# Optimization experiments

Measured on AMD Instinct MI355X. Metric: run time of the kernel, lower is better.

Reference implementation:

```python
import jax, jax.numpy as jnp
import numpy as np

B, N, E, D, H, C, FF, NQ, NCLS = 4, 1024, 512, 256, 2, 128, 1024, 4, 24
K_LOCAL, K_GLOBAL = 8, 7


def _ln(x, g, b, eps=1e-5):
    m = jnp.mean(x, -1, keepdims=True)
    v = jnp.mean((x - m) ** 2, -1, keepdims=True)
    return (x - m) * jax.lax.rsqrt(v + eps) * g + b


def _knn_mask(dist, k, exclude_self):
    # dist: [n, n]; returns bool mask[target, source] of k nearest sources per target
    n = dist.shape[-1]
    d = jnp.where(jnp.eye(n, dtype=bool), 1e9, dist) if exclude_self else dist
    idx = jax.lax.top_k(-d, k)[1]  # [n, k]
    rows = jnp.arange(n)[:, None]
    return jnp.zeros((n, n), dtype=bool).at[rows, idx].set(True)


def _mha(q, k, v, scale, extra_mask=None):
    # q: [B,Lq,H,C]  k,v: [B,Lk,H,C]
    logits = jnp.einsum('bqhc,bkhc->bhqk', q, k) * scale
    if extra_mask is not None:
        logits = logits + extra_mask
    a = jax.nn.softmax(logits, axis=-1)
    return jnp.einsum('bhqk,bkhc->bqhc', a, v)


def _forward(inputs, cellposes, sparse_rand, emb_W, emb_b, pe_tab, pe_W1, pe_b1, pe_W2, pe_b2,
             gat_W, gat_att_src, gat_att_dst, gat_b, ln_g, ln_b,
             tf_qkv_W, tf_qkv_b, tf_out_W, tf_out_b, tf_ff1_W, tf_ff1_b, tf_ff2_W, tf_ff2_b,
             tf_ln1_g, tf_ln1_b, tf_ln2_g, tf_ln2_b,
             query_embed, pool_in_W, pool_in_b, pool_out_W, pool_out_b,
             m1_W, m1_b, m_ln1_g, m_ln1_b, m2_W, m2_b, m_ln2_g, m_ln2_b, m3_W, m3_b,
             c1_W, c1_b, c2_W, c2_b, c3_W, c3_b, c4_W, c4_b, masks):
    # masks are all ones (full bags) -> key_padding_mask is all-False, no padding effect
    x = inputs @ emb_W.T + emb_b                                  # [B,N,D]
    # 2D position embedding: per-coordinate Embedding -> Linear -> ReLU -> Linear
    pos_idx = jnp.clip(cellposes, 0, 1000).astype(jnp.int32)      # [B,N,2]
    pes = []
    for c in range(2):
        e = pe_tab[c][pos_idx[..., c]]                            # [B,N,D//2]
        e = jax.nn.relu(e @ pe_W1[c].T + pe_b1[c]) @ pe_W2[c].T + pe_b2[c]
        pes.append(e)
    x = x + jnp.concatenate(pes, axis=-1)
    # kNN graph: local k=8 with self-loops + global k=7 without; coalesce('max') => edge-set union
    pm = cellposes.mean(axis=1, keepdims=True)
    ps = cellposes.std(axis=1, keepdims=True) + 1e-8
    pn = (cellposes - pm) / ps
    sq = jnp.sum((pn[:, :, None, :] - pn[:, None, :, :]) ** 2, axis=-1)
    dist = jax.lax.stop_gradient(jnp.sqrt(sq + 1e-12))            # [B,N,N]
    local = jax.vmap(lambda d: _knn_mask(d, K_LOCAL, False))(dist)
    glob = jax.vmap(lambda d: _knn_mask(d, K_GLOBAL, True))(dist)
    adj = local | glob                                            # [B, target, source]
    # GAT layers (PyG GATConv; edge weights are ignored since edge_dim=None)
    for l in range(gat_W.shape[0]):
        res = x
        h = (x @ gat_W[l].T).reshape(B, N, H, C)
        a_src = jnp.einsum('bnhc,hc->bnh', h, gat_att_src[l])
        a_dst = jnp.einsum('bnhc,hc->bnh', h, gat_att_dst[l])
        e = jax.nn.leaky_relu(a_dst[:, :, None, :] + a_src[:, None, :, :], 0.2)  # [B,t,s,H]
        e = jnp.where(adj[..., None], e, -1e9)
        a = jax.nn.softmax(e, axis=2)
        out = jnp.einsum('btsh,bshc->bthc', a, h).reshape(B, N, D) + gat_b[l]
        x = _ln(out + res, ln_g, ln_b)
    # TransformerEncoder: post-norm, ReLU FFN, batch_first, eval (no dropout)
    scale = 1.0 / jnp.sqrt(jnp.float32(C))
    for l in range(tf_qkv_W.shape[0]):
        qkv = x @ tf_qkv_W[l].T + tf_qkv_b[l]
        q, k, v = [t.reshape(B, N, H, C) for t in jnp.split(qkv, 3, axis=-1)]
        o = _mha(q, k, v, scale).reshape(B, N, D) @ tf_out_W[l].T + tf_out_b[l]
        x = _ln(x + o, tf_ln1_g[l], tf_ln1_b[l])
        ff = jax.nn.relu(x @ tf_ff1_W[l].T + tf_ff1_b[l]) @ tf_ff2_W[l].T + tf_ff2_b[l]
        x = _ln(x + ff, tf_ln2_g[l], tf_ln2_b[l])
    x = _ln(x, ln_g, ln_b)
    pooled_avg = x.mean(axis=1)                                   # AdaptiveAvgPool1d(1) == mean over seq
    # Sparse multihead attention pooling with learned queries
    queries = jnp.broadcast_to(query_embed[None], (B, NQ, D))
    attn_mask = jnp.where(sparse_rand < 0.3, 0.0, -1e9)           # [NQ, N]
    Wq, Wk, Wv = jnp.split(pool_in_W, 3, axis=0)
    bq, bk, bv = jnp.split(pool_in_b, 3, axis=0)
    q = (queries @ Wq.T + bq).reshape(B, NQ, H, C)
    k = (x @ Wk.T + bk).reshape(B, N, H, C)
    v = (x @ Wv.T + bv).reshape(B, N, H, C)
    pooled_att = _mha(q, k, v, scale, attn_mask[None, None]).reshape(B, NQ, D) @ pool_out_W.T + pool_out_b
    combined = jnp.concatenate([pooled_avg, pooled_att.reshape(B, NQ * D)], axis=-1)  # [B,(1+NQ)*D]
    h = jax.nn.relu(combined @ m1_W.T + m1_b)
    h = _ln(h, m_ln1_g, m_ln1_b)
    h = jax.nn.relu(h @ m2_W.T + m2_b)
    h = _ln(h, m_ln2_g, m_ln2_b)
    h = h @ m3_W.T + m3_b
    h = jax.nn.relu(h @ c1_W.T + c1_b)
    h = jax.nn.relu(h @ c2_W.T + c2_b)
    h = jax.nn.relu(h @ c3_W.T + c3_b)
    return h @ c4_W.T + c4_b                                      # [B, num_classes]


def setup_inputs() -> dict:
    key = jax.random.key(0)
    ks = iter(jax.random.split(key, 80))
    def W(shape, s=0.02):
        return jax.random.normal(next(ks), shape, jnp.float32) * s
    z = lambda *s: jnp.zeros(s, jnp.float32)
    o = lambda *s: jnp.ones(s, jnp.float32)
    return dict(
        inputs=jax.random.normal(next(ks), (B, N, E), jnp.float32),
        cellposes=jax.random.uniform(next(ks), (B, N, 2), jnp.float32) * 1000.0,
        sparse_rand=jax.random.uniform(next(ks), (NQ, N), jnp.float32),
        emb_W=W((D, E)), emb_b=z(D),
        pe_tab=W((2, 1001, D // 2)), pe_W1=W((2, D // 2, D // 2)), pe_b1=z(2, D // 2),
        pe_W2=W((2, D // 2, D // 2)), pe_b2=z(2, D // 2),
        gat_W=W((2, D, D)), gat_att_src=W((2, H, C)), gat_att_dst=W((2, H, C)), gat_b=z(2, D),
        ln_g=o(D), ln_b=z(D),
        tf_qkv_W=W((2, 3 * D, D)), tf_qkv_b=z(2, 3 * D), tf_out_W=W((2, D, D)), tf_out_b=z(2, D),
        tf_ff1_W=W((2, FF, D)), tf_ff1_b=z(2, FF), tf_ff2_W=W((2, D, FF)), tf_ff2_b=z(2, D),
        tf_ln1_g=o(2, D), tf_ln1_b=z(2, D), tf_ln2_g=o(2, D), tf_ln2_b=z(2, D),
        query_embed=W((NQ, D)),
        pool_in_W=W((3 * D, D)), pool_in_b=z(3 * D), pool_out_W=W((D, D)), pool_out_b=z(D),
        m1_W=W((1024, (1 + NQ) * D)), m1_b=z(1024), m_ln1_g=o(1024), m_ln1_b=z(1024),
        m2_W=W((1024, 1024)), m2_b=z(1024), m_ln2_g=o(1024), m_ln2_b=z(1024),
        m3_W=W((1024, 1024)), m3_b=z(1024),
        c1_W=W((1032, 1024)), c1_b=z(1032), c2_W=W((512, 1032)), c2_b=z(512),
        c3_W=W((256, 512)), c3_b=z(256), c4_W=W((NCLS, 256)), c4_b=z(NCLS),
        masks=jnp.ones((B, N), jnp.int32),
    )


def reference(inputs, cellposes, sparse_rand, emb_W, emb_b, pe_tab, pe_W1, pe_b1, pe_W2, pe_b2,
              gat_W, gat_att_src, gat_att_dst, gat_b, ln_g, ln_b,
              tf_qkv_W, tf_qkv_b, tf_out_W, tf_out_b, tf_ff1_W, tf_ff1_b, tf_ff2_W, tf_ff2_b,
              tf_ln1_g, tf_ln1_b, tf_ln2_g, tf_ln2_b,
              query_embed, pool_in_W, pool_in_b, pool_out_W, pool_out_b,
              m1_W, m1_b, m_ln1_g, m_ln1_b, m2_W, m2_b, m_ln2_g, m_ln2_b, m3_W, m3_b,
              c1_W, c1_b, c2_W, c2_b, c3_W, c3_b, c4_W, c4_b, masks):
    return _forward(inputs, cellposes, sparse_rand, emb_W, emb_b, pe_tab, pe_W1, pe_b1, pe_W2, pe_b2,
                    gat_W, gat_att_src, gat_att_dst, gat_b, ln_g, ln_b,
                    tf_qkv_W, tf_qkv_b, tf_out_W, tf_out_b, tf_ff1_W, tf_ff1_b, tf_ff2_W, tf_ff2_b,
                    tf_ln1_g, tf_ln1_b, tf_ln2_g, tf_ln2_b,
                    query_embed, pool_in_W, pool_in_b, pool_out_W, pool_out_b,
                    m1_W, m1_b, m_ln1_g, m_ln1_b, m2_W, m2_b, m_ln2_g, m_ln2_b, m3_W, m3_b,
                    c1_W, c1_b, c2_W, c2_b, c3_W, c3_b, c4_W, c4_b, masks)
```

## Files before the change

kernel.cpp:

```cpp
#include <hip/hip_runtime.h>
#include <hip/hip_bf16.h>


typedef __bf16 bf16x8 __attribute__((ext_vector_type(8)));
typedef float  f32x4  __attribute__((ext_vector_type(4)));

__device__ __forceinline__ ushort f2b(float f) {
  __hip_bfloat16 h = __float2bfloat16(f);
  return *(ushort*)&h;
}
__device__ __forceinline__ float b2f(ushort u) {
  union { unsigned i; float f; } v; v.i = ((unsigned)u) << 16; return v.f;
}

__device__ __forceinline__ float blk_sum256(float v, float* red) {
  int t = threadIdx.x;
  red[t] = v; __syncthreads();
  #pragma unroll
  for (int off = 128; off > 0; off >>= 1) {
    if (t < off) red[t] += red[t + off];
    __syncthreads();
  }
  float r = red[0]; __syncthreads();
  return r;
}

__device__ __forceinline__ void stage8(const ushort* __restrict__ src, ushort* dst) {
  *(uint4*)dst = *(const uint4*)src;
}
__device__ __forceinline__ void stage8(const float* __restrict__ src, ushort* dst) {
  float4 a = ((const float4*)src)[0];
  float4 b = ((const float4*)src)[1];
  ushort4 o0, o1;
  o0.x = f2b(a.x); o0.y = f2b(a.y); o0.z = f2b(a.z); o0.w = f2b(a.w);
  o1.x = f2b(b.x); o1.y = f2b(b.y); o1.z = f2b(b.z); o1.w = f2b(b.w);
  *(ushort4*)dst = o0;
  *(ushort4*)(dst + 4) = o1;
}

template<typename CT, typename AT, typename WT, bool VSPLIT, bool GATS>
__global__ __launch_bounds__(256) void mfma_gemm(
    const AT* __restrict__ A, int lda,
    const WT* __restrict__ Bw, int ldb,
    const float* __restrict__ bias,
    CT* __restrict__ C, int ldc, int K, int relu,
    ushort* __restrict__ VT,
    const float* __restrict__ asrcW, const float* __restrict__ adstW,
    float* __restrict__ ASRC, float* __restrict__ ADST)
{
  __shared__ ushort As[64][40];
  __shared__ ushort Bs[128][40];
  int tid = threadIdx.x;
  int lane = tid & 63, wave = tid >> 6;
  int wm = wave >> 1, wn = wave & 1;
  int quad = lane >> 4, l16 = lane & 15;
  long mBase = blockIdx.y * 64, nBase = blockIdx.x * 128;

  f32x4 zero4 = {0.f, 0.f, 0.f, 0.f};
  f32x4 acc[2][4];
  #pragma unroll
  for (int i = 0; i < 2; i++)
    #pragma unroll
    for (int j = 0; j < 4; j++) acc[i][j] = zero4;

  for (int k0 = 0; k0 < K; k0 += 32) {
    {
      int r = tid >> 2, sg = (tid & 3) * 8;
      stage8(A + (mBase + r) * lda + k0 + sg, &As[r][sg]);
    }
    #pragma unroll
    for (int p = 0; p < 2; p++) {
      int idx = p * 256 + tid;
      int r = idx >> 2, sg = (idx & 3) * 8;
      stage8(Bw + (nBase + r) * ldb + k0 + sg, &Bs[r][sg]);
    }
    __syncthreads();
    bf16x8 af[2], bfr[4];
    #pragma unroll
    for (int i = 0; i < 2; i++)
      af[i] = *(const bf16x8*)&As[wm * 32 + i * 16 + l16][quad * 8];
    #pragma unroll
    for (int j = 0; j < 4; j++)
      bfr[j] = *(const bf16x8*)&Bs[wn * 64 + j * 16 + l16][quad * 8];
    #pragma unroll
    for (int i = 0; i < 2; i++)
      #pragma unroll
      for (int j = 0; j < 4; j++)
        acc[i][j] = __builtin_amdgcn_mfma_f32_16x16x32_bf16(af[i], bfr[j], acc[i][j], 0, 0, 0);
    __syncthreads();
  }
  #pragma unroll
  for (int i = 0; i < 2; i++) {
    #pragma unroll
    for (int j = 0; j < 4; j++) {
      long col = nBase + wn * 64 + j * 16 + l16;
      float bv = bias ? bias[col] : 0.f;
      long row0 = mBase + wm * 32 + i * 16 + quad * 4;
      if (VSPLIT && col >= 512) {
        int cm = (int)col - 512, hh = cm >> 7, cc = cm & 127;
        long bidx = row0 >> 10, n0 = row0 & 1023;
        ushort4 o;
        o.x = f2b(acc[i][j][0] + bv);
        o.y = f2b(acc[i][j][1] + bv);
        o.z = f2b(acc[i][j][2] + bv);
        o.w = f2b(acc[i][j][3] + bv);
        *(ushort4*)&VT[(((bidx * 2 + hh) * 128 + cc) << 10) + n0] = o;
      } else {
        #pragma unroll
        for (int r = 0; r < 4; r++) {
          float v = acc[i][j][r] + bv;
          if (relu) v = fmaxf(v, 0.f);
          if constexpr (sizeof(CT) == 2) C[(row0 + r) * ldc + col] = f2b(v);
          else                           C[(row0 + r) * ldc + col] = v;
        }
      }
    }
  }
  if constexpr (GATS) {
    __shared__ float RS[64][2], RD[64][2];
    float ps[2][4], pd[2][4];
    #pragma unroll
    for (int i = 0; i < 2; i++)
      #pragma unroll
      for (int r = 0; r < 4; r++) { ps[i][r] = 0.f; pd[i][r] = 0.f; }
    #pragma unroll
    for (int j = 0; j < 4; j++) {
      long col = nBase + wn * 64 + j * 16 + l16;
      float ws = asrcW[col], wd = adstW[col];
      #pragma unroll
      for (int i = 0; i < 2; i++)
        #pragma unroll
        for (int r = 0; r < 4; r++) {
          ps[i][r] += acc[i][j][r] * ws;
          pd[i][r] += acc[i][j][r] * wd;
        }
    }
    #pragma unroll
    for (int off = 1; off < 16; off <<= 1)
      #pragma unroll
      for (int i = 0; i < 2; i++)
        #pragma unroll
        for (int r = 0; r < 4; r++) {
          ps[i][r] += __shfl_xor(ps[i][r], off);
          pd[i][r] += __shfl_xor(pd[i][r], off);
        }
    if (l16 == 0) {
      #pragma unroll
      for (int i = 0; i < 2; i++)
        #pragma unroll
        for (int r = 0; r < 4; r++) {
          int row = wm * 32 + i * 16 + quad * 4 + r;
          RS[row][wn] = ps[i][r];
          RD[row][wn] = pd[i][r];
        }
    }
    __syncthreads();
    if (tid < 64) {
      long gr = mBase + tid;
      ASRC[gr * 2 + blockIdx.x] = RS[tid][0] + RS[tid][1];
      ADST[gr * 2 + blockIdx.x] = RD[tid][0] + RD[tid][1];
    }
  }
}

template<typename CT, typename AT, typename WT>
static void mgemm(hipStream_t st, const AT* A, int lda, const WT* B, int ldb,
                  const float* bias, CT* C, int ldc, int M, int N, int K, int relu) {
  dim3 grid(N / 128, M / 64);
  mfma_gemm<CT, AT, WT, false, false><<<grid, 256, 0, st>>>(
      A, lda, B, ldb, bias, C, ldc, K, relu, nullptr, nullptr, nullptr, nullptr, nullptr);
}
template<typename AT, typename WT>
static void mgemm_vt(hipStream_t st, const AT* A, int lda, const WT* B, int ldb,
                     const float* bias, ushort* C, int ldc, int M, int N, int K, ushort* VT) {
  dim3 grid(N / 128, M / 64);
  mfma_gemm<ushort, AT, WT, true, false><<<grid, 256, 0, st>>>(
      A, lda, B, ldb, bias, C, ldc, K, 0, VT, nullptr, nullptr, nullptr, nullptr);
}
template<typename AT, typename WT>
static void mgemm_gat(hipStream_t st, const AT* A, int lda, const WT* B, int ldb,
                      float* C, int ldc, int M, int N, int K,
                      const float* asrcW, const float* adstW, float* AS, float* AD) {
  dim3 grid(N / 128, M / 64);
  mfma_gemm<float, AT, WT, false, true><<<grid, 256, 0, st>>>(
      A, lda, B, ldb, nullptr, C, ldc, K, 0, nullptr, asrcW, adstW, AS, AD);
}

__global__ __launch_bounds__(256) void pos_mlp(
    const float* __restrict__ cellp, const float* __restrict__ tab,
    const float* __restrict__ W1, const float* __restrict__ b1,
    const float* __restrict__ W2, const float* __restrict__ b2,
    float* __restrict__ X, ushort* __restrict__ Xb)
{
  __shared__ ushort Es[64][136];
  __shared__ ushort Bs[128][136];
  __shared__ ushort H1s[64][136];
  int tid = threadIdx.x;
  int lane = tid & 63, wave = tid >> 6;
  int wm = wave >> 1, wn = wave & 1;
  int quad = lane >> 4, l16 = lane & 15;
  int r0 = blockIdx.x * 64, c = blockIdx.y;

  #pragma unroll
  for (int p = 0; p < 4; p++) {
    int idx = p * 256 + tid;
    int r = idx >> 4, c8 = (idx & 15) * 8;
    float pos = cellp[(r0 + r) * 2 + c];
    pos = fminf(fmaxf(pos, 0.f), 1000.f);
    int pi = (int)pos;
    stage8(tab + ((long)(c * 1001 + pi)) * 128 + c8, &Es[r][c8]);
  }
  #pragma unroll
  for (int p = 0; p < 8; p++) {
    int idx = p * 256 + tid;
    int r = idx >> 4, c8 = (idx & 15) * 8;
    stage8(W1 + ((long)(c * 128 + r)) * 128 + c8, &Bs[r][c8]);
  }
  __syncthreads();

  f32x4 zero4 = {0.f, 0.f, 0.f, 0.f};
  f32x4 acc[2][4];
  #pragma unroll
  for (int i = 0; i < 2; i++)
    #pragma unroll
    for (int j = 0; j < 4; j++) acc[i][j] = zero4;
  #pragma unroll
  for (int ks = 0; ks < 4; ks++) {
    bf16x8 af[2], bfr[4];
    #pragma unroll
    for (int i = 0; i < 2; i++)
      af[i] = *(const bf16x8*)&Es[wm * 32 + i * 16 + l16][ks * 32 + quad * 8];
    #pragma unroll
    for (int j = 0; j < 4; j++)
      bfr[j] = *(const bf16x8*)&Bs[wn * 64 + j * 16 + l16][ks * 32 + quad * 8];
    #pragma unroll
    for (int i = 0; i < 2; i++)
      #pragma unroll
      for (int j = 0; j < 4; j++)
        acc[i][j] = __builtin_amdgcn_mfma_f32_16x16x32_bf16(af[i], bfr[j], acc[i][j], 0, 0, 0);
  }
  #pragma unroll
  for (int i = 0; i < 2; i++)
    #pragma unroll
    for (int j = 0; j < 4; j++) {
      int col = wn * 64 + j * 16 + l16;
      float bv = b1[c * 128 + col];
      #pragma unroll
      for (int r = 0; r < 4; r++) {
        int row = wm * 32 + i * 16 + quad * 4 + r;
        H1s[row][col] = f2b(fmaxf(acc[i][j][r] + bv, 0.f));
      }
    }
  __syncthreads();
  #pragma unroll
  for (int p = 0; p < 8; p++) {
    int idx = p * 256 + tid;
    int r = idx >> 4, c8 = (idx & 15) * 8;
    stage8(W2 + ((long)(c * 128 + r)) * 128 + c8, &Bs[r][c8]);
  }
  __syncthreads();
  #pragma unroll
  for (int i = 0; i < 2; i++)
    #pragma unroll
    for (int j = 0; j < 4; j++) acc[i][j] = zero4;
  #pragma unroll
  for (int ks = 0; ks < 4; ks++) {
    bf16x8 af[2], bfr[4];
    #pragma unroll
    for (int i = 0; i < 2; i++)
      af[i] = *(const bf16x8*)&H1s[wm * 32 + i * 16 + l16][ks * 32 + quad * 8];
    #pragma unroll
    for (int j = 0; j < 4; j++)
      bfr[j] = *(const bf16x8*)&Bs[wn * 64 + j * 16 + l16][ks * 32 + quad * 8];
    #pragma unroll
    for (int i = 0; i < 2; i++)
      #pragma unroll
      for (int j = 0; j < 4; j++)
        acc[i][j] = __builtin_amdgcn_mfma_f32_16x16x32_bf16(af[i], bfr[j], acc[i][j], 0, 0, 0);
  }
  #pragma unroll
  for (int i = 0; i < 2; i++)
    #pragma unroll
    for (int j = 0; j < 4; j++) {
      int col = wn * 64 + j * 16 + l16;
      float bv = b2[c * 128 + col];
      #pragma unroll
      for (int r = 0; r < 4; r++) {
        long row = r0 + wm * 32 + i * 16 + quad * 4 + r;
        long idx = row * 256 + c * 128 + col;
        float v = X[idx] + (acc[i][j][r] + bv);
        X[idx] = v;
        Xb[idx] = f2b(v);
      }
    }
}

template<int M_>
__global__ __launch_bounds__(256) void skinny_gemm(
    const float* __restrict__ A, int lda,
    const float* __restrict__ W, int K,
    float* __restrict__ P, int N, int slice)
{
  __shared__ float Asl[M_ * 192];
  __shared__ float Pr[4][M_][64];
  int tid = threadIdx.x;
  int ks = blockIdx.y;
  int kbeg = ks * slice;
  int kend = min(K, kbeg + slice);
  int sl = kend - kbeg;
  for (int idx = tid; idx < M_ * sl; idx += 256) {
    int m = idx / sl, k = idx - m * sl;
    Asl[m * sl + k] = A[(long)m * lda + kbeg + k];
  }
  __syncthreads();
  int n = blockIdx.x * 64 + (tid & 63);
  int sub = tid >> 6;
  int sl4 = (sl + 3) >> 2;
  int k0 = kbeg + sub * sl4;
  int k1 = min(kend, k0 + sl4);
  float acc[M_];
  #pragma unroll
  for (int m = 0; m < M_; m++) acc[m] = 0.f;
  if (n < N) {
    const float* wr = W + (long)n * K;
    for (int k = k0; k < k1; k++) {
      float w = wr[k];
      int kl = k - kbeg;
      #pragma unroll
      for (int m = 0; m < M_; m++) acc[m] += w * Asl[m * sl + kl];
    }
  }
  #pragma unroll
  for (int m = 0; m < M_; m++) Pr[sub][m][tid & 63] = acc[m];
  __syncthreads();
  if (sub == 0 && n < N) {
    #pragma unroll
    for (int m = 0; m < M_; m++) {
      float s = Pr[0][m][tid] + Pr[1][m][tid] + Pr[2][m][tid] + Pr[3][m][tid];
      P[((long)(ks * M_ + m)) * N + n] = s;
    }
  }
}

__global__ __launch_bounds__(256) void skinny_epi(
    const float* __restrict__ P, const float* __restrict__ bias,
    float* __restrict__ out, int M, int N, int KS, int relu)
{
  int idx = blockIdx.x * 256 + threadIdx.x;
  if (idx >= M * N) return;
  int m = idx / N, n = idx - m * N;
  float s = bias[n];
  for (int ks = 0; ks < KS; ks++) s += P[((long)(ks * M + m)) * N + n];
  if (relu) s = fmaxf(s, 0.f);
  out[(long)m * N + n] = s;
}

template<int M_>
static void sgemm(hipStream_t st, const float* A, int lda, const float* W, int K,
                  const float* bias, float* out, float* P, int N, int KS, int relu) {
  int slice = (K + KS - 1) / KS;
  dim3 grid((N + 63) / 64, KS);
  skinny_gemm<M_><<<grid, 256, 0, st>>>(A, lda, W, K, P, N, slice);
  skinny_epi<<<(M_ * N + 255) / 256, 256, 0, st>>>(P, bias, out, M_, N, KS, relu);
}

__device__ __forceinline__ void merge8(float* D, int* I,
                                       const float* cd, const int* ci, int stride) {
  #pragma unroll 1
  for (int j = 0; j < 8; j++) {
    float d = cd[j * stride]; int idx = ci[j * stride];
    bool better = (d < D[7]) || (d == D[7] && idx < I[7]);
    if (!better) break;
    D[7] = d; I[7] = idx;
    #pragma unroll
    for (int p = 7; p > 0; p--) {
      bool sw = (D[p] < D[p - 1]) || (D[p] == D[p - 1] && I[p] < I[p - 1]);
      if (sw) {
        float td = D[p]; D[p] = D[p - 1]; D[p - 1] = td;
        int ti = I[p]; I[p] = I[p - 1]; I[p - 1] = ti;
      }
    }
  }
}

__global__ __launch_bounds__(256) void knn_fused(const float* __restrict__ cellp,
                                                 int* __restrict__ NBR) {
  int blk = blockIdx.x;
  int b = blk >> 7, grp = blk & 127;
  int tid = threadIdx.x;
  int tl = tid >> 5, chunk = tid & 31;
  __shared__ float px[1024], py[1024];
  __shared__ float red[256];
  __shared__ float candD[8][8][32];
  __shared__ int   candI[8][8][32];
  for (int i = tid; i < 1024; i += 256) {
    px[i] = cellp[((b << 10) + i) * 2 + 0];
    py[i] = cellp[((b << 10) + i) * 2 + 1];
  }
  __syncthreads();
  float s = 0.f;
  for (int n = tid; n < 1024; n += 256) s += px[n];
  float meanx = blk_sum256(s, red) * (1.f / 1024.f);
  s = 0.f;
  for (int n = tid; n < 1024; n += 256) { float d = px[n] - meanx; s += d * d; }
  float invx = 1.f / (sqrtf(blk_sum256(s, red) * (1.f / 1024.f)) + 1e-8f);
  s = 0.f;
  for (int n = tid; n < 1024; n += 256) s += py[n];
  float meany = blk_sum256(s, red) * (1.f / 1024.f);
  s = 0.f;
  for (int n = tid; n < 1024; n += 256) { float d = py[n] - meany; s += d * d; }
  float invy = 1.f / (sqrtf(blk_sum256(s, red) * (1.f / 1024.f)) + 1e-8f);
  for (int n = tid; n < 1024; n += 256) {
    px[n] = (px[n] - meanx) * invx;
    py[n] = (py[n] - meany) * invy;
  }
  __syncthreads();
  int t = grp * 8 + tl;
  float tx = px[t], ty = py[t];
  float d8[8]; int i8[8];
  #pragma unroll
  for (int i = 0; i < 8; i++) { d8[i] = 3.4e38f; i8[i] = 0x7fffffff; }
  for (int ss = chunk; ss < 1024; ss += 32) {
    float dx = __fadd_rn(px[ss], -tx), dy = __fadd_rn(py[ss], -ty);
    float d2 = __fadd_rn(__fadd_rn(__fmul_rn(dx, dx), __fmul_rn(dy, dy)), 1e-12f);
    float d = sqrtf(d2);
    if (d < d8[7]) {
      d8[7] = d; i8[7] = ss;
      #pragma unroll
      for (int p = 7; p > 0; p--) {
        if (d8[p] < d8[p - 1]) {
          float td = d8[p]; d8[p] = d8[p - 1]; d8[p - 1] = td;
          int ti = i8[p]; i8[p] = i8[p - 1]; i8[p - 1] = ti;
        }
      }
    }
  }
  #pragma unroll
  for (int i = 0; i < 8; i++) { candD[tl][i][chunk] = d8[i]; candI[tl][i][chunk] = i8[i]; }
  __syncthreads();
  if ((chunk & 7) == 0) {
    float D[8]; int I[8];
    #pragma unroll
    for (int i = 0; i < 8; i++) { D[i] = candD[tl][i][chunk]; I[i] = candI[tl][i][chunk]; }
    for (int c = chunk + 1; c < chunk + 8; c++)
      merge8(D, I, &candD[tl][0][c], &candI[tl][0][c], 32);
    #pragma unroll
    for (int i = 0; i < 8; i++) { candD[tl][i][chunk] = D[i]; candI[tl][i][chunk] = I[i]; }
  }
  __syncthreads();
  if (chunk == 0) {
    float D[8]; int I[8];
    #pragma unroll
    for (int i = 0; i < 8; i++) { D[i] = candD[tl][i][0]; I[i] = candI[tl][i][0]; }
    merge8(D, I, &candD[tl][0][8], &candI[tl][0][8], 32);
    merge8(D, I, &candD[tl][0][16], &candI[tl][0][16], 32);
    merge8(D, I, &candD[tl][0][24], &candI[tl][0][24], 32);
    #pragma unroll
    for (int i = 0; i < 8; i++) NBR[((long)((b << 10) + t)) * 8 + i] = I[i];
  }
}

__global__ __launch_bounds__(256) void gat_aggr_ln(
    const float* __restrict__ Hh, const float* __restrict__ ASRC, const float* __restrict__ ADST,
    const int* __restrict__ NBR, const float* __restrict__ gbias,
    const float* __restrict__ lng, const float* __restrict__ lnb,
    float* __restrict__ X, ushort* __restrict__ Xb)
{
  int row = blockIdx.x, tid = threadIdx.x;
  int b = row >> 10;
  __shared__ int nb[8];
  __shared__ float w[2][8];
  __shared__ float red[256];
  if (tid < 8) {
    int v = NBR[(long)row * 8 + tid];
    nb[tid] = min(max(v, 0), 1023);
  }
  __syncthreads();
  if (tid < 16) {
    int i = tid & 7, h = tid >> 3;
    float e = ADST[row * 2 + h] + ASRC[((b << 10) + nb[i]) * 2 + h];
    w[h][i] = (e >= 0.f) ? e : 0.2f * e;
  }
  __syncthreads();
  if (tid < 2) {
    float m = -3.4e38f;
    for (int i = 0; i < 8; i++) m = fmaxf(m, w[tid][i]);
    float s = 0.f;
    for (int i = 0; i < 8; i++) { float e = expf(w[tid][i] - m); w[tid][i] = e; s += e; }
    float inv = 1.f / s;
    for (int i = 0; i < 8; i++) w[tid][i] *= inv;
  }
  __syncthreads();
  int h = tid >> 7, c = tid & 127;
  float acc = 0.f;
  #pragma unroll
  for (int i = 0; i < 8; i++)
    acc += w[h][i] * Hh[((long)((b << 10) + nb[i])) * 256 + h * 128 + c];
  float v = acc + gbias[tid] + X[(long)row * 256 + tid];
  float mean = blk_sum256(v, red) * (1.f / 256.f);
  float dv = v - mean;
  float var = blk_sum256(dv * dv, red) * (1.f / 256.f);
  float o = dv * rsqrtf(var + 1e-5f) * lng[tid] + lnb[tid];
  X[(long)row * 256 + tid] = o;
  Xb[(long)row * 256 + tid] = f2b(o);
}

__global__ __launch_bounds__(256) void add_ln4(const float* __restrict__ res,
    const float* __restrict__ Yv, const float* __restrict__ g, const float* __restrict__ b,
    float* __restrict__ out, ushort* __restrict__ outb)
{
  int wave = threadIdx.x >> 6, lane = threadIdx.x & 63;
  long row = blockIdx.x * 4 + wave;
  const float* yr = Yv + row * 256;
  const float* rr = res ? res + row * 256 : nullptr;
  float v[4];
  float s = 0.f;
  #pragma unroll
  for (int i = 0; i < 4; i++) {
    int d = lane + i * 64;
    float x = yr[d];
    if (rr) x += rr[d];
    v[i] = x; s += x;
  }
  #pragma unroll
  for (int off = 32; off > 0; off >>= 1) s += __shfl_xor(s, off);
  float mean = s * (1.f / 256.f);
  float vs = 0.f;
  #pragma unroll
  for (int i = 0; i < 4; i++) { float dv = v[i] - mean; vs += dv * dv; }
  #pragma unroll
  for (int off = 32; off > 0; off >>= 1) vs += __shfl_xor(vs, off);
  float rstd = rsqrtf(vs * (1.f / 256.f) + 1e-5f);
  #pragma unroll
  for (int i = 0; i < 4; i++) {
    int d = lane + i * 64;
    float o = (v[i] - mean) * rstd * g[d] + b[d];
    out[row * 256 + d] = o;
    if (outb) outb[row * 256 + d] = f2b(o);
  }
}

__global__ __launch_bounds__(256) void add_ln_big(const float* __restrict__ Yv,
    const float* __restrict__ g, const float* __restrict__ b,
    float* __restrict__ out)
{
  int row = blockIdx.x, tid = threadIdx.x;
  __shared__ float red[256];
  float vals[4];
  float s = 0.f;
  #pragma unroll
  for (int i = 0; i < 4; i++) {
    int d = tid + (i << 8);
    float v = Yv[(long)row * 1024 + d];
    vals[i] = v; s += v;
  }
  float mean = blk_sum256(s, red) * (1.f / 1024.f);
  s = 0.f;
  #pragma unroll
  for (int i = 0; i < 4; i++) { float dv = vals[i] - mean; s += dv * dv; }
  float var = blk_sum256(s, red) * (1.f / 1024.f);
  float rstd = rsqrtf(var + 1e-5f);
  #pragma unroll
  for (int i = 0; i < 4; i++) {
    int d = tid + (i << 8);
    out[(long)row * 1024 + d] = (vals[i] - mean) * rstd * g[d] + b[d];
  }
}

__global__ __launch_bounds__(256) void flash_mfma(const ushort* __restrict__ QKV,
                                                  const ushort* __restrict__ VT,
                                                  ushort* __restrict__ O)
{
  const float scale = 0.08838834764831845f;
  int blk = blockIdx.x;
  int qt = blk & 15, bh = blk >> 4;
  int b = bh >> 1, h = bh & 1;
  const ushort* qkg = QKV + (long)b * 1024 * 768 + h * 128;
  const ushort* vtg = VT + ((long)bh << 17);

  __shared__ ushort Qs[64][136];
  __shared__ ushort Ks[64][136];
  __shared__ ushort Vt[128][72];
  __shared__ ushort Ps[4][16][72];

  int tid = threadIdx.x;
  int wave = tid >> 6, lane = tid & 63;
  int quad = lane >> 4, l16 = lane & 15;

  #pragma unroll
  for (int p = 0; p < 4; p++) {
    int idx = p * 256 + tid;
    int r = idx >> 4, c8 = (idx & 15) * 8;
    *(uint4*)&Qs[r][c8] = *(const uint4*)(qkg + (long)(qt * 64 + r) * 768 + c8);
  }
  __syncthreads();
  bf16x8 af[4];
  #pragma unroll
  for (int ks = 0; ks < 4; ks++)
    af[ks] = *(const bf16x8*)&Qs[wave * 16 + l16][ks * 32 + quad * 8];

  f32x4 Oacc[8];
  f32x4 zero4 = {0.f, 0.f, 0.f, 0.f};
  #pragma unroll
  for (int j = 0; j < 8; j++) Oacc[j] = zero4;
  float mr[4], lr[4];
  #pragma unroll
  for (int r = 0; r < 4; r++) { mr[r] = -3.4e38f; lr[r] = 0.f; }

  for (int kt = 0; kt < 16; kt++) {
    __syncthreads();
    #pragma unroll
    for (int p = 0; p < 4; p++) {
      int idx = p * 256 + tid;
      int r = idx >> 4, c8 = (idx & 15) * 8;
      *(uint4*)&Ks[r][c8] = *(const uint4*)(qkg + (long)(kt * 64 + r) * 768 + 256 + c8);
      int c = idx >> 3, k8 = (idx & 7) * 8;
      *(uint4*)&Vt[c][k8] = *(const uint4*)(vtg + ((long)c << 10) + kt * 64 + k8);
    }
    __syncthreads();
    f32x4 acc[4];
    #pragma unroll
    for (int j = 0; j < 4; j++) acc[j] = zero4;
    #pragma unroll
    for (int ks = 0; ks < 4; ks++) {
      #pragma unroll
      for (int j = 0; j < 4; j++) {
        bf16x8 kb = *(const bf16x8*)&Ks[j * 16 + l16][ks * 32 + quad * 8];
        acc[j] = __builtin_amdgcn_mfma_f32_16x16x32_bf16(af[ks], kb, acc[j], 0, 0, 0);
      }
    }
    float sv[4][4], tmax[4];
    #pragma unroll
    for (int r = 0; r < 4; r++) tmax[r] = -3.4e38f;
    #pragma unroll
    for (int j = 0; j < 4; j++)
      #pragma unroll
      for (int r = 0; r < 4; r++) {
        float x = acc[j][r] * scale;
        sv[j][r] = x;
        tmax[r] = fmaxf(tmax[r], x);
      }
    #pragma unroll
    for (int off = 1; off < 16; off <<= 1)
      #pragma unroll
      for (int r = 0; r < 4; r++) tmax[r] = fmaxf(tmax[r], __shfl_xor(tmax[r], off));
    float alpha[4], rsum[4];
    #pragma unroll
    for (int r = 0; r < 4; r++) {
      float mn = fmaxf(mr[r], tmax[r]);
      alpha[r] = expf(mr[r] - mn);
      mr[r] = mn;
      rsum[r] = 0.f;
    }
    #pragma unroll
    for (int j = 0; j < 4; j++)
      #pragma unroll
      for (int r = 0; r < 4; r++) {
        float p = expf(sv[j][r] - mr[r]);
        sv[j][r] = p;
        rsum[r] += p;
      }
    #pragma unroll
    for (int off = 1; off < 16; off <<= 1)
      #pragma unroll
      for (int r = 0; r < 4; r++) rsum[r] += __shfl_xor(rsum[r], off);
    #pragma unroll
    for (int r = 0; r < 4; r++) lr[r] = lr[r] * alpha[r] + rsum[r];
    #pragma unroll
    for (int j = 0; j < 4; j++)
      #pragma unroll
      for (int r = 0; r < 4; r++)
        Ps[wave][quad * 4 + r][j * 16 + l16] = f2b(sv[j][r]);
    #pragma unroll
    for (int jj = 0; jj < 8; jj++)
      #pragma unroll
      for (int r = 0; r < 4; r++) Oacc[jj][r] *= alpha[r];
    __syncthreads();
    #pragma unroll
    for (int s = 0; s < 2; s++) {
      bf16x8 pa = *(const bf16x8*)&Ps[wave][l16][s * 32 + quad * 8];
      #pragma unroll
      for (int jj = 0; jj < 8; jj++) {
        bf16x8 vb = *(const bf16x8*)&Vt[jj * 16 + l16][s * 32 + quad * 8];
        Oacc[jj] = __builtin_amdgcn_mfma_f32_16x16x32_bf16(pa, vb, Oacc[jj], 0, 0, 0);
      }
    }
  }
  long row0 = (long)b * 1024 + qt * 64 + wave * 16 + quad * 4;
  #pragma unroll
  for (int jj = 0; jj < 8; jj++) {
    int col = h * 128 + jj * 16 + l16;
    #pragma unroll
    for (int r = 0; r < 4; r++)
      O[(row0 + r) * 256 + col] = f2b(Oacc[jj][r] / lr[r]);
  }
}

__global__ __launch_bounds__(128) void pool_split(
    const float* __restrict__ qe, const float* __restrict__ pinW, const float* __restrict__ pinB,
    const float* __restrict__ srand, const ushort* __restrict__ KV,
    float* __restrict__ PM, float* __restrict__ PL, float* __restrict__ PO)
{
  int cid = blockIdx.x;
  int id = blockIdx.y;
  int h = id & 1, nq = (id >> 1) & 3, b = id >> 3;
  int tid = threadIdx.x;
  __shared__ float qs[128];
  __shared__ float eg[128];
  __shared__ float red[128];
  {
    float a = pinB[h * 128 + tid];
    const float* wr = pinW + ((long)(h * 128 + tid)) * 256;
    const float* qr = qe + nq * 256;
    for (int i = 0; i < 256; i++) a += qr[i] * wr[i];
    qs[tid] = a;
  }
  __syncthreads();
  const float scale = 0.08838834764831845f;
  int s = cid * 128 + tid;
  float d = 0.f;
  {
    const ushort* kr = KV + ((long)((b << 10) + s)) * 512 + h * 128;
    #pragma unroll
    for (int c8 = 0; c8 < 128; c8 += 8) {
      uint4 kv4 = *(const uint4*)(kr + c8);
      const ushort* kp = (const ushort*)&kv4;
      #pragma unroll
      for (int j = 0; j < 8; j++) d += qs[c8 + j] * b2f(kp[j]);
    }
  }
  float lg = d * scale + ((srand[nq * 1024 + s] < 0.3f) ? 0.f : -1e9f);
  red[tid] = lg; __syncthreads();
  for (int off = 64; off > 0; off >>= 1) { if (tid < off) red[tid] = fmaxf(red[tid], red[tid + off]); __syncthreads(); }
  float m = red[0]; __syncthreads();
  float e = expf(lg - m);
  eg[tid] = e;
  red[tid] = e; __syncthreads();
  for (int off = 64; off > 0; off >>= 1) { if (tid < off) red[tid] += red[tid + off]; __syncthreads(); }
  float l = red[0];
  __syncthreads();
  float o = 0.f;
  const ushort* vbase = KV + ((long)((b << 10) + cid * 128)) * 512 + 256 + h * 128 + tid;
  for (int ss = 0; ss < 128; ss++)
    o += eg[ss] * b2f(vbase[(long)ss * 512]);
  int part = id * 8 + cid;
  PO[(long)part * 128 + tid] = o;
  if (tid == 0) { PM[part] = m; PL[part] = l; }
}

__global__ __launch_bounds__(128) void pool_merge(
    const float* __restrict__ PM, const float* __restrict__ PL, const float* __restrict__ PO,
    float* __restrict__ ATTP)
{
  int id = blockIdx.x;
  int h = id & 1, nq = (id >> 1) & 3, b = id >> 3;
  int tid = threadIdx.x;
  float m = -3.4e38f;
  #pragma unroll
  for (int c = 0; c < 8; c++) m = fmaxf(m, PM[id * 8 + c]);
  float l = 0.f, o = 0.f;
  #pragma unroll
  for (int c = 0; c < 8; c++) {
    float w = expf(PM[id * 8 + c] - m);
    l += PL[id * 8 + c] * w;
    o += PO[(long)(id * 8 + c) * 128 + tid] * w;
  }
  ATTP[(b * 4 + nq) * 256 + h * 128 + tid] = o / l;
}

__global__ __launch_bounds__(256) void col_mean_part(const float* __restrict__ X,
                                                     float* __restrict__ PSUM)
{
  int blk = blockIdx.x;
  int b = blk >> 4, ch = blk & 15;
  int d = threadIdx.x;
  float s = 0.f;
  int n0 = ch * 64;
  const float* xr = X + ((long)((b << 10) + n0)) * 256 + d;
  #pragma unroll 4
  for (int n = 0; n < 64; n++) s += xr[(long)n * 256];
  PSUM[(long)blk * 256 + d] = s;
}

__global__ __launch_bounds__(256) void combined_merge(const float* __restrict__ PSUM,
    const float* __restrict__ ATTO, float* __restrict__ CMB)
{
  int b = blockIdx.x, d = threadIdx.x;
  float s = 0.f;
  #pragma unroll
  for (int ch = 0; ch < 16; ch++) s += PSUM[(long)(b * 16 + ch) * 256 + d];
  CMB[b * 1280 + d] = s * (1.f / 1024.f);
  #pragma unroll
  for (int q = 0; q < 4; q++)
    CMB[b * 1280 + 256 + q * 256 + d] = ATTO[(b * 4 + q) * 256 + d];
}

__global__ void store_out(const float* __restrict__ src, float* __restrict__ dst, int n) {
  int i = blockIdx.x * blockDim.x + threadIdx.x;
  if (i < n) dst[i] = src[i];
}
__global__ void fill_out_zero(float* __restrict__ dst, int n) {
  int i = blockIdx.x * blockDim.x + threadIdx.x;
  if (i < n) dst[i] = 0.f;
}

extern "C" void kernel_launch(void* const* d_in, const int* in_sizes, int n_in,
                              void* d_out, int out_size, void* d_ws, size_t ws_size,
                              hipStream_t stream)
{
  const float* inp      = (const float*)d_in[0];
  const float* cellp    = (const float*)d_in[1];
  const float* srand    = (const float*)d_in[2];
  const float* emb_W    = (const float*)d_in[3];
  const float* emb_b    = (const float*)d_in[4];
  const float* pe_tab   = (const float*)d_in[5];
  const float* pe_W1    = (const float*)d_in[6];
  const float* pe_b1    = (const float*)d_in[7];
  const float* pe_W2    = (const float*)d_in[8];
  const float* pe_b2    = (const float*)d_in[9];
  const float* gat_W    = (const float*)d_in[10];
  const float* gat_asrc = (const float*)d_in[11];
  const float* gat_adst = (const float*)d_in[12];
  const float* gat_b    = (const float*)d_in[13];
  const float* ln_g     = (const float*)d_in[14];
  const float* ln_b     = (const float*)d_in[15];
  const float* qkv_W    = (const float*)d_in[16];
  const float* qkv_b    = (const float*)d_in[17];
  const float* out_W    = (const float*)d_in[18];
  const float* out_b    = (const float*)d_in[19];
  const float* ff1_W    = (const float*)d_in[20];
  const float* ff1_b    = (const float*)d_in[21];
  const float* ff2_W    = (const float*)d_in[22];
  const float* ff2_b    = (const float*)d_in[23];
  const float* ln1_g    = (const float*)d_in[24];
  const float* ln1_b    = (const float*)d_in[25];
  const float* ln2_g    = (const float*)d_in[26];
  const float* ln2_b    = (const float*)d_in[27];
  const float* q_emb    = (const float*)d_in[28];
  const float* pin_W    = (const float*)d_in[29];
  const float* pin_b    = (const float*)d_in[30];
  const float* pout_W   = (const float*)d_in[31];
  const float* pout_b   = (const float*)d_in[32];
  const float* m1_W     = (const float*)d_in[33];
  const float* m1_b     = (const float*)d_in[34];
  const float* mln1_g   = (const float*)d_in[35];
  const float* mln1_b   = (const float*)d_in[36];
  const float* m2_W     = (const float*)d_in[37];
  const float* m2_b     = (const float*)d_in[38];
  const float* mln2_g   = (const float*)d_in[39];
  const float* mln2_b   = (const float*)d_in[40];
  const float* m3_W     = (const float*)d_in[41];
  const float* m3_b     = (const float*)d_in[42];
  const float* c1_W     = (const float*)d_in[43];
  const float* c1_b     = (const float*)d_in[44];
  const float* c2_W     = (const float*)d_in[45];
  const float* c2_b     = (const float*)d_in[46];
  const float* c3_W     = (const float*)d_in[47];
  const float* c3_b     = (const float*)d_in[48];
  const float* c4_W     = (const float*)d_in[49];
  const float* c4_b     = (const float*)d_in[50];
  (void)in_sizes; (void)n_in;

  char* base = (char*)d_ws;
  size_t off = 0;
  auto alloc = [&](size_t bytes) { void* p = base + off; off += (bytes + 255) & ~size_t(255); return p; };
  float* AS    = (float*)alloc(32768);
  float* AD    = (float*)alloc(32768);
  float* ATTP  = (float*)alloc(16384);
  float* ATTO  = (float*)alloc(16384);
  float* CMB   = (float*)alloc(20480);
  float* Ha    = (float*)alloc(16384);
  float* Hb    = (float*)alloc(16384);
  float* Hc    = (float*)alloc(16640);
  float* Hd    = (float*)alloc(8192);
  float* He    = (float*)alloc(4096);
  float* Hf    = (float*)alloc(512);
  float* Pk    = (float*)alloc(262144);
  float* PPM   = (float*)alloc(1024);
  float* PPL   = (float*)alloc(1024);
  float* PPO   = (float*)alloc(131072);
  float* PSUM  = (float*)alloc(65536);
  int*   NBR   = (int*)alloc(131072);
  float* X     = (float*)alloc(4194304);
  ushort* Xb   = (ushort*)alloc(2097152);
  char*  Rq    = (char*)alloc(6291456);
  char*  Rf    = (char*)alloc(4194304);
  float*  F1   = (float*)alloc(4194304);
  ushort* QKVb = (ushort*)Rq;
  float*  F2   = (float*)Rq;
  ushort* KVb  = (ushort*)Rq;
  ushort* Ob   = (ushort*)Rf;
  ushort* VT   = (ushort*)(Rf + 2097152);
  ushort* FFBb = (ushort*)Rf;
  if (ws_size < off) { fill_out_zero<<<1, 128, 0, stream>>>((float*)d_out, out_size); return; }

  knn_fused<<<512, 256, 0, stream>>>(cellp, NBR);

  mgemm<float>(stream, inp, 512, emb_W, 512, emb_b, X, 256, 4096, 256, 512, 0);
  pos_mlp<<<dim3(64, 2), 256, 0, stream>>>(cellp, pe_tab, pe_W1, pe_b1, pe_W2, pe_b2, X, Xb);

  for (int l = 0; l < 2; l++) {
    mgemm_gat(stream, Xb, 256, gat_W + l * 65536, 256, F1, 256, 4096, 256, 256,
              gat_asrc + l * 256, gat_adst + l * 256, AS, AD);
    gat_aggr_ln<<<4096, 256, 0, stream>>>(F1, AS, AD, NBR, gat_b + l * 256, ln_g, ln_b, X, Xb);
  }

  for (int l = 0; l < 2; l++) {
    mgemm_vt(stream, Xb, 256, qkv_W + (long)l * 768 * 256, 256, qkv_b + l * 768,
             QKVb, 768, 4096, 768, 256, VT);
    flash_mfma<<<256, 256, 0, stream>>>(QKVb, VT, Ob);
    mgemm<float>(stream, Ob, 256, out_W + l * 65536, 256, out_b + l * 256, F2, 256,
                 4096, 256, 256, 0);
    add_ln4<<<1024, 256, 0, stream>>>(X, F2, ln1_g + l * 256, ln1_b + l * 256, X, Xb);
    mgemm<ushort>(stream, Xb, 256, ff1_W + l * 262144, 256, ff1_b + l * 1024,
                  FFBb, 1024, 4096, 1024, 256, 1);
    mgemm<float>(stream, FFBb, 1024, ff2_W + l * 262144, 1024, ff2_b + l * 256,
                 F2, 256, 4096, 256, 1024, 0);
    add_ln4<<<1024, 256, 0, stream>>>(X, F2, ln2_g + l * 256, ln2_b + l * 256, X, Xb);
  }

  add_ln4<<<1024, 256, 0, stream>>>((const float*)nullptr, X, ln_g, ln_b, X, Xb);

  mgemm<ushort>(stream, Xb, 256, pin_W + 65536, 256, pin_b + 256, KVb, 512, 4096, 512, 256, 0);
  pool_split<<<dim3(8, 32), 128, 0, stream>>>(q_emb, pin_W, pin_b, srand, KVb, PPM, PPL, PPO);
  pool_merge<<<32, 128, 0, stream>>>(PPM, PPL, PPO, ATTP);
  sgemm<16>(stream, ATTP, 256, pout_W, 256, pout_b, ATTO, Pk, 256, 2, 0);
  col_mean_part<<<64, 256, 0, stream>>>(X, PSUM);
  combined_merge<<<4, 256, 0, stream>>>(PSUM, ATTO, CMB);

  sgemm<4>(stream, CMB, 1280, m1_W, 1280, m1_b, Ha, Pk, 1024, 8, 1);
  add_ln_big<<<4, 256, 0, stream>>>(Ha, mln1_g, mln1_b, Ha);
  sgemm<4>(stream, Ha, 1024, m2_W, 1024, m2_b, Hb, Pk, 1024, 8, 1);
  add_ln_big<<<4, 256, 0, stream>>>(Hb, mln2_g, mln2_b, Hb);
  sgemm<4>(stream, Hb, 1024, m3_W, 1024, m3_b, Ha, Pk, 1024, 8, 0);
  sgemm<4>(stream, Ha, 1024, c1_W, 1024, c1_b, Hc, Pk, 1032, 8, 1);
  sgemm<4>(stream, Hc, 1032, c2_W, 1032, c2_b, Hd, Pk, 512, 8, 1);
  sgemm<4>(stream, Hd, 512, c3_W, 512, c3_b, He, Pk, 256, 4, 1);
  sgemm<4>(stream, He, 256, c4_W, 256, c4_b, Hf, Pk, 24, 2, 0);
  store_out<<<1, 128, 0, stream>>>(Hf, (float*)d_out, out_size);
}
```

Measured before the change: 664.5 us.

## Split kNN into per-bag stats kernel and wave-shuffle top-8 selection

Per-bag coordinate normalization moves into a separate small kernel, so the 512 kNN blocks no longer each recompute mean and std with many block-wide reductions. The kNN selection now gives one 64-lane wave per target, keeps 16 distances per lane, and pulls out the top 8 with eight wave-wide 64-bit min shuffle reductions. This replaces the per-thread insertion sort and the shared-memory merge tree. The cost is an extra kernel launch and a round trip through global memory for the normalized coordinates.

```diff
diff --git a/kernel.cpp b/kernel.cpp
--- a/kernel.cpp
+++ b/kernel.cpp
@@ -364,99 +364,65 @@
   skinny_epi<<<(M_ * N + 255) / 256, 256, 0, st>>>(P, bias, out, M_, N, KS, relu);
 }
 
-__device__ __forceinline__ void merge8(float* D, int* I,
-                                       const float* cd, const int* ci, int stride) {
-  #pragma unroll 1
-  for (int j = 0; j < 8; j++) {
-    float d = cd[j * stride]; int idx = ci[j * stride];
-    bool better = (d < D[7]) || (d == D[7] && idx < I[7]);
-    if (!better) break;
-    D[7] = d; I[7] = idx;
-    #pragma unroll
-    for (int p = 7; p > 0; p--) {
-      bool sw = (D[p] < D[p - 1]) || (D[p] == D[p - 1] && I[p] < I[p - 1]);
-      if (sw) {
-        float td = D[p]; D[p] = D[p - 1]; D[p - 1] = td;
-        int ti = I[p]; I[p] = I[p - 1]; I[p - 1] = ti;
-      }
-    }
-  }
-}
-
-__global__ __launch_bounds__(256) void knn_fused(const float* __restrict__ cellp,
-                                                 int* __restrict__ NBR) {
+__global__ __launch_bounds__(256) void bag_stats(const float* __restrict__ cp, float* __restrict__ PN) {
+  int b = blockIdx.x, tid = threadIdx.x;
+  __shared__ float red[256];
+  for (int c = 0; c < 2; c++) {
+    float s = 0.f;
+    for (int n = tid; n < 1024; n += 256) s += cp[((b << 10) + n) * 2 + c];
+    float mean = blk_sum256(s, red) * (1.f / 1024.f);
+    s = 0.f;
+    for (int n = tid; n < 1024; n += 256) { float d = cp[((b << 10) + n) * 2 + c] - mean; s += d * d; }
+    float var = blk_sum256(s, red) * (1.f / 1024.f);
+    float inv = 1.f / (sqrtf(var) + 1e-8f);
+    for (int n = tid; n < 1024; n += 256)
+      PN[((b << 10) + n) * 2 + c] = (cp[((b << 10) + n) * 2 + c] - mean) * inv;
+  }
+}
+
+__global__ __launch_bounds__(256) void knn_sel(const float* __restrict__ PN,
+                                               int* __restrict__ NBR) {
   int blk = blockIdx.x;
   int b = blk >> 7, grp = blk & 127;
   int tid = threadIdx.x;
-  int tl = tid >> 5, chunk = tid & 31;
+  int wave = tid >> 6, lane = tid & 63;
   __shared__ float px[1024], py[1024];
-  __shared__ float red[256];
-  __shared__ float candD[8][8][32];
-  __shared__ int   candI[8][8][32];
   for (int i = tid; i < 1024; i += 256) {
-    px[i] = cellp[((b << 10) + i) * 2 + 0];
-    py[i] = cellp[((b << 10) + i) * 2 + 1];
-  }
-  __syncthreads();
-  float s = 0.f;
-  for (int n = tid; n < 1024; n += 256) s += px[n];
-  float meanx = blk_sum256(s, red) * (1.f / 1024.f);
-  s = 0.f;
-  for (int n = tid; n < 1024; n += 256) { float d = px[n] - meanx; s += d * d; }
-  float invx = 1.f / (sqrtf(blk_sum256(s, red) * (1.f / 1024.f)) + 1e-8f);
-  s = 0.f;
-  for (int n = tid; n < 1024; n += 256) s += py[n];
-  float meany = blk_sum256(s, red) * (1.f / 1024.f);
-  s = 0.f;
-  for (int n = tid; n < 1024; n += 256) { float d = py[n] - meany; s += d * d; }
-  float invy = 1.f / (sqrtf(blk_sum256(s, red) * (1.f / 1024.f)) + 1e-8f);
-  for (int n = tid; n < 1024; n += 256) {
-    px[n] = (px[n] - meanx) * invx;
-    py[n] = (py[n] - meany) * invy;
-  }
-  __syncthreads();
-  int t = grp * 8 + tl;
-  float tx = px[t], ty = py[t];
-  float d8[8]; int i8[8];
-  #pragma unroll
-  for (int i = 0; i < 8; i++) { d8[i] = 3.4e38f; i8[i] = 0x7fffffff; }
-  for (int ss = chunk; ss < 1024; ss += 32) {
-    float dx = __fadd_rn(px[ss], -tx), dy = __fadd_rn(py[ss], -ty);
-    float d2 = __fadd_rn(__fadd_rn(__fmul_rn(dx, dx), __fmul_rn(dy, dy)), 1e-12f);
-    float d = sqrtf(d2);
-    if (d < d8[7]) {
-      d8[7] = d; i8[7] = ss;
-      #pragma unroll
-      for (int p = 7; p > 0; p--) {
-        if (d8[p] < d8[p - 1]) {
-          float td = d8[p]; d8[p] = d8[p - 1]; d8[p - 1] = td;
-          int ti = i8[p]; i8[p] = i8[p - 1]; i8[p - 1] = ti;
-        }
+    px[i] = PN[((b << 10) + i) * 2 + 0];
+    py[i] = PN[((b << 10) + i) * 2 + 1];
+  }
+  __syncthreads();
+  #pragma unroll
+  for (int sub = 0; sub < 2; sub++) {
+    int t = grp * 8 + wave * 2 + sub;
+    float tx = px[t], ty = py[t];
+    float dloc[16];
+    #pragma unroll
+    for (int k = 0; k < 16; k++) {
+      int s = lane + (k << 6);
+      float dx = __fadd_rn(px[s], -tx), dy = __fadd_rn(py[s], -ty);
+      float d2 = __fadd_rn(__fadd_rn(__fmul_rn(dx, dx), __fmul_rn(dy, dy)), 1e-12f);
+      dloc[k] = sqrtf(d2);
+    }
+    int res[8];
+    #pragma unroll
+    for (int it = 0; it < 8; it++) {
+      float bd = dloc[0]; int bk = 0;
+      #pragma unroll
+      for (int k = 1; k < 16; k++)
+        if (dloc[k] < bd) { bd = dloc[k]; bk = k; }
+      unsigned long long key =
+          (((unsigned long long)__float_as_uint(bd)) << 32) | (unsigned)(lane + (bk << 6));
+      #pragma unroll
+      for (int off = 1; off < 64; off <<= 1) {
+        unsigned long long o = __shfl_xor(key, off);
+        if (o < key) key = o;
       }
-    }
-  }
-  #pragma unroll
-  for (int i = 0; i < 8; i++) { candD[tl][i][chunk] = d8[i]; candI[tl][i][chunk] = i8[i]; }
-  __syncthreads();
-  if ((chunk & 7) == 0) {
-    float D[8]; int I[8];
-    #pragma unroll
-    for (int i = 0; i < 8; i++) { D[i] = candD[tl][i][chunk]; I[i] = candI[tl][i][chunk]; }
-    for (int c = chunk + 1; c < chunk + 8; c++)
-      merge8(D, I, &candD[tl][0][c], &candI[tl][0][c], 32);
-    #pragma unroll
-    for (int i = 0; i < 8; i++) { candD[tl][i][chunk] = D[i]; candI[tl][i][chunk] = I[i]; }
-  }
-  __syncthreads();
-  if (chunk == 0) {
-    float D[8]; int I[8];
-    #pragma unroll
-    for (int i = 0; i < 8; i++) { D[i] = candD[tl][i][0]; I[i] = candI[tl][i][0]; }
-    merge8(D, I, &candD[tl][0][8], &candI[tl][0][8], 32);
-    merge8(D, I, &candD[tl][0][16], &candI[tl][0][16], 32);
-    merge8(D, I, &candD[tl][0][24], &candI[tl][0][24], 32);
-    #pragma unroll
-    for (int i = 0; i < 8; i++) NBR[((long)((b << 10) + t)) * 8 + i] = I[i];
+      int widx = (int)(key & 0xffffffffu);
+      res[it] = widx;
+      if ((widx & 63) == lane) dloc[widx >> 6] = 3.4e38f;
+    }
+    if (lane < 8) NBR[((long)((b << 10) + t)) * 8 + lane] = res[lane];
   }
 }
 
@@ -864,6 +830,7 @@
   char* base = (char*)d_ws;
   size_t off = 0;
   auto alloc = [&](size_t bytes) { void* p = base + off; off += (bytes + 255) & ~size_t(255); return p; };
+  float* PN    = (float*)alloc(32768);
   float* AS    = (float*)alloc(32768);
   float* AD    = (float*)alloc(32768);
   float* ATTP  = (float*)alloc(16384);
@@ -894,7 +861,8 @@
   ushort* FFBb = (ushort*)Rf;
   if (ws_size < off) { fill_out_zero<<<1, 128, 0, stream>>>((float*)d_out, out_size); return; }
 
-  knn_fused<<<512, 256, 0, stream>>>(cellp, NBR);
+  bag_stats<<<4, 256, 0, stream>>>(cellp, PN);
+  knn_sel<<<512, 256, 0, stream>>>(PN, NBR);
 
   mgemm<float>(stream, inp, 512, emb_W, 512, emb_b, X, 256, 4096, 256, 512, 0);
   pos_mlp<<<dim3(64, 2), 256, 0, stream>>>(cellp, pe_tab, pe_W1, pe_b1, pe_W2, pe_b2, X, Xb);
```

Result: faster. 622.0 us (-6.4%).
